# Performance work log

Measured on AMD Instinct MI355X. Metric: run time of the kernel, lower is better.

Reference implementation:

```python
import jax, jax.numpy as jnp
import numpy as np

T, N, H = 256, 64, 512
DT, GAMMA, EPS = 0.01, 1.0, 1.0

def setup_inputs() -> dict:
    key = jax.random.key(0)
    ks = jax.random.split(key, 6)
    s = 1.0 / np.sqrt(H)  # keep recurrent dynamics stable
    return {
        "x": jax.random.normal(ks[0], (T, N, H), jnp.float32),
        "connection_matrix": (jax.random.uniform(ks[1], (N, N)) < 0.5).astype(jnp.float32),
        "W_h": jax.random.normal(ks[2], (N, H, H), jnp.float32) * s,
        "W_x": jax.random.normal(ks[3], (N, H, H), jnp.float32) * s,
        "b": jax.random.normal(ks[4], (N, H), jnp.float32) * 0.1,
        "initial_states": jnp.zeros((N, 2, H), jnp.float32),
    }

def reference(x, connection_matrix, W_h, W_x, b, initial_states):
    # x: (T, N, H); states: (N, 2, H) with states[:,0] = h_y (the archetype output)
    def step(carry, x_t):
        states, outs = carry
        # message passing: mix previous outputs through the connection matrix,
        # then gate with the external input (elementwise)
        new_ins = (connection_matrix @ outs) * x_t                      # (N, H)
        hy, hz = states[:, 0], states[:, 1]
        # batched RON cell over all N archetypes
        pre = (jnp.einsum('nij,nj->ni', W_h, hy)
               + jnp.einsum('nij,nj->ni', W_x, new_ins) + b)            # (N, H)
        hz_n = hz + DT * (jnp.tanh(pre) - GAMMA * hy - EPS * hz)
        hy_n = hy + DT * hz_n
        new_states = jnp.stack([hy_n, hz_n], axis=1)                    # (N, 2, H)
        return (new_states, hy_n), (new_states, new_ins)

    init_outs = jnp.zeros_like(x[0])  # initial_outs=None path in the original
    _, (states_seq, ins_seq) = jax.lax.scan(step, (initial_states, init_outs), x)
    # original prepends the initial state and x[0] to the returned lists
    states_all = jnp.concatenate([initial_states[None], states_seq], axis=0)  # (T+1, N, 2, H)
    ins_all = jnp.concatenate([x[:1], ins_seq], axis=0)                       # (T+1, N, H)
    return states_all, ins_all
```

## Files before the change

kernel.cpp:

```cpp
#include <hip/hip_runtime.h>
#include <hip/hip_cooperative_groups.h>

namespace cg = cooperative_groups;

constexpr int   T_     = 256;
constexpr int   N_     = 64;
constexpr int   H_     = 512;
constexpr float DT_    = 0.01f;
constexpr float GAMMA_ = 1.0f;
constexpr float EPS_   = 1.0f;

constexpr int GRID  = 1024;
constexpr int BLOCK = 256;
constexpr int WGPN  = GRID / N_;
constexpr int ROWS  = H_ / WGPN;
constexpr int RPW   = ROWS / 4;
constexpr int LROWS = 16;

__global__ __launch_bounds__(BLOCK, 4)
void archetypes_persistent(const float* __restrict__ x,
                           const float* __restrict__ conn,
                           const float* __restrict__ W_h,
                           const float* __restrict__ W_x,
                           const float* __restrict__ bias,
                           const float* __restrict__ init_states,
                           float* __restrict__ out)
{
    cg::grid_group grid = cg::this_grid();

    const int tid  = threadIdx.x;
    const int wg   = blockIdx.x;
    const int n    = wg / WGPN;
    const int q    = wg % WGPN;
    const int lane = tid & 63;
    const int wave = tid >> 6;

    float* states_all = out;
    float* ins_all    = out + (size_t)(T_ + 1) * N_ * 2 * H_;

    __shared__ float s_hy[H_];
    __shared__ float s_ins[H_];
    __shared__ float s_pre[ROWS];
    __shared__ float s_conn[N_];
    __shared__ float s_bias[ROWS];
    __shared__ float s_wx[LROWS][H_];

    const float4* Wh4 = (const float4*)(W_h + ((size_t)n * H_ + q * ROWS) * H_);
    const float4* Wx4 = (const float4*)(W_x + ((size_t)n * H_ + q * ROWS) * H_);
    float4 wh_reg[RPW][2];
    #pragma unroll
    for (int j = 0; j < RPW; ++j) {
        const int r_l = wave + 4 * j;
        #pragma unroll
        for (int k = 0; k < 2; ++k)
            wh_reg[j][k] = Wh4[r_l * (H_ / 4) + k * 64 + lane];
    }
    {
        float4* dst = (float4*)&s_wx[0][0];
        for (int idx = tid; idx < LROWS * H_ / 4; idx += BLOCK)
            dst[idx] = Wx4[idx];
    }
    if (tid < N_)   s_conn[tid] = conn[n * N_ + tid];
    if (tid < ROWS) s_bias[tid] = bias[n * H_ + q * ROWS + tid];

    for (int idx = wg * BLOCK + tid; idx < N_ * 2 * H_; idx += GRID * BLOCK)
        states_all[idx] = init_states[idx];
    for (int idx = wg * BLOCK + tid; idx < N_ * H_; idx += GRID * BLOCK)
        ins_all[idx] = x[idx];

    grid.sync();

    for (int t = 0; t < T_; ++t) {
        const float* st_t = states_all + (size_t)t * N_ * 2 * H_;

        {
            const int h0 = tid, h1 = tid + 256;
            float i0 = 0.f, i1 = 0.f;
            if (t > 0) {
                const float* xr = x + (size_t)t * N_ * H_ + n * H_;
                float a0 = 0.f, a1 = 0.f;
                #pragma unroll 8
                for (int m = 0; m < N_; ++m) {
                    const float c = s_conn[m];
                    a0 += c * st_t[m * 2 * H_ + h0];
                    a1 += c * st_t[m * 2 * H_ + h1];
                }
                i0 = a0 * xr[h0];
                i1 = a1 * xr[h1];
            }
            s_ins[h0] = i0;
            s_ins[h1] = i1;
            s_hy[h0] = st_t[n * 2 * H_ + h0];
            s_hy[h1] = st_t[n * 2 * H_ + h1];
            float* insd = ins_all + (size_t)(t + 1) * N_ * H_ + n * H_;
            if (h0 / ROWS == q) insd[h0] = i0;
            if (h1 / ROWS == q) insd[h1] = i1;
        }
        __syncthreads();

        {
            const float4* vh = (const float4*)s_hy;
            const float4* vi = (const float4*)s_ins;
            const float4 v0 = vh[lane], v1 = vh[64 + lane];
            const float4 u0 = vi[lane], u1 = vi[64 + lane];
            #pragma unroll
            for (int j = 0; j < RPW; ++j) {
                const int r_l = wave + 4 * j;
                float4 wx0, wx1;
                if (j < 4) {
                    const float4* lx = (const float4*)&s_wx[r_l][0];
                    wx0 = lx[lane];
                    wx1 = lx[64 + lane];
                } else {
                    wx0 = Wx4[r_l * (H_ / 4) + lane];
                    wx1 = Wx4[r_l * (H_ / 4) + 64 + lane];
                }
                float acc = 0.f;
                acc += wh_reg[j][0].x * v0.x + wh_reg[j][0].y * v0.y +
                       wh_reg[j][0].z * v0.z + wh_reg[j][0].w * v0.w;
                acc += wx0.x * u0.x + wx0.y * u0.y + wx0.z * u0.z + wx0.w * u0.w;
                acc += wh_reg[j][1].x * v1.x + wh_reg[j][1].y * v1.y +
                       wh_reg[j][1].z * v1.z + wh_reg[j][1].w * v1.w;
                acc += wx1.x * u1.x + wx1.y * u1.y + wx1.z * u1.z + wx1.w * u1.w;
                #pragma unroll
                for (int off = 32; off; off >>= 1)
                    acc += __shfl_xor(acc, off);
                if (lane == 0) s_pre[r_l] = acc;
            }
        }
        __syncthreads();

        if (tid < ROWS) {
            const int i   = q * ROWS + tid;
            const float pre  = s_pre[tid] + s_bias[tid];
            const float hy   = st_t[n * 2 * H_ + i];
            const float hz   = st_t[n * 2 * H_ + H_ + i];
            const float th   = tanhf(pre);
            const float hz_n = hz + DT_ * (th - GAMMA_ * hy - EPS_ * hz);
            const float hy_n = hy + DT_ * hz_n;
            float* st1 = states_all + (size_t)(t + 1) * N_ * 2 * H_ + n * 2 * H_;
            st1[i]      = hy_n;
            st1[H_ + i] = hz_n;
        }

        grid.sync();
    }
}

__global__ __launch_bounds__(BLOCK)
void archetypes_init(const float* __restrict__ x,
                     const float* __restrict__ init_states,
                     float* __restrict__ out)
{
    float* states_all = out;
    float* ins_all    = out + (size_t)(T_ + 1) * N_ * 2 * H_;
    const int idx = blockIdx.x * BLOCK + threadIdx.x;
    if (idx < N_ * 2 * H_) states_all[idx] = init_states[idx];
    if (idx < N_ * H_)     ins_all[idx]    = x[idx];
}

__global__ __launch_bounds__(BLOCK)
void archetypes_step(int t,
                     const float* __restrict__ x,
                     const float* __restrict__ conn,
                     const float* __restrict__ W_h,
                     const float* __restrict__ W_x,
                     const float* __restrict__ bias,
                     float* __restrict__ out)
{
    const int tid  = threadIdx.x;
    const int wg   = blockIdx.x;
    const int n    = wg / WGPN;
    const int q    = wg % WGPN;
    const int lane = tid & 63;
    const int wave = tid >> 6;

    float* states_all = out;
    float* ins_all    = out + (size_t)(T_ + 1) * N_ * 2 * H_;

    __shared__ float s_hy[H_];
    __shared__ float s_ins[H_];
    __shared__ float s_pre[ROWS];
    __shared__ float s_conn[N_];
    __shared__ float s_bias[ROWS];

    if (tid < N_)   s_conn[tid] = conn[n * N_ + tid];
    if (tid < ROWS) s_bias[tid] = bias[n * H_ + q * ROWS + tid];
    __syncthreads();

    const float* st_t = states_all + (size_t)t * N_ * 2 * H_;
    {
        const int h0 = tid, h1 = tid + 256;
        float i0 = 0.f, i1 = 0.f;
        if (t > 0) {
            const float* xr = x + (size_t)t * N_ * H_ + n * H_;
            float a0 = 0.f, a1 = 0.f;
            #pragma unroll 8
            for (int m = 0; m < N_; ++m) {
                const float c = s_conn[m];
                a0 += c * st_t[m * 2 * H_ + h0];
                a1 += c * st_t[m * 2 * H_ + h1];
            }
            i0 = a0 * xr[h0];
            i1 = a1 * xr[h1];
        }
        s_ins[h0] = i0;
        s_ins[h1] = i1;
        s_hy[h0] = st_t[n * 2 * H_ + h0];
        s_hy[h1] = st_t[n * 2 * H_ + h1];
        float* insd = ins_all + (size_t)(t + 1) * N_ * H_ + n * H_;
        if (h0 / ROWS == q) insd[h0] = i0;
        if (h1 / ROWS == q) insd[h1] = i1;
    }
    __syncthreads();
    {
        const float4* vh = (const float4*)s_hy;
        const float4* vi = (const float4*)s_ins;
        const float4* Wh4 = (const float4*)(W_h + ((size_t)n * H_ + q * ROWS) * H_);
        const float4* Wx4 = (const float4*)(W_x + ((size_t)n * H_ + q * ROWS) * H_);
        const float4 v0 = vh[lane], v1 = vh[64 + lane];
        const float4 u0 = vi[lane], u1 = vi[64 + lane];
        #pragma unroll
        for (int j = 0; j < RPW; ++j) {
            const int r_l = wave + 4 * j;
            const float4 a0 = Wh4[r_l * (H_ / 4) + lane];
            const float4 a1 = Wh4[r_l * (H_ / 4) + 64 + lane];
            const float4 wx0 = Wx4[r_l * (H_ / 4) + lane];
            const float4 wx1 = Wx4[r_l * (H_ / 4) + 64 + lane];
            float acc = 0.f;
            acc += a0.x * v0.x + a0.y * v0.y + a0.z * v0.z + a0.w * v0.w;
            acc += wx0.x * u0.x + wx0.y * u0.y + wx0.z * u0.z + wx0.w * u0.w;
            acc += a1.x * v1.x + a1.y * v1.y + a1.z * v1.z + a1.w * v1.w;
            acc += wx1.x * u1.x + wx1.y * u1.y + wx1.z * u1.z + wx1.w * u1.w;
            #pragma unroll
            for (int off = 32; off; off >>= 1)
                acc += __shfl_xor(acc, off);
            if (lane == 0) s_pre[r_l] = acc;
        }
    }
    __syncthreads();
    if (tid < ROWS) {
        const int i   = q * ROWS + tid;
        const float pre  = s_pre[tid] + s_bias[tid];
        const float hy   = st_t[n * 2 * H_ + i];
        const float hz   = st_t[n * 2 * H_ + H_ + i];
        const float th   = tanhf(pre);
        const float hz_n = hz + DT_ * (th - GAMMA_ * hy - EPS_ * hz);
        const float hy_n = hy + DT_ * hz_n;
        float* st1 = states_all + (size_t)(t + 1) * N_ * 2 * H_ + n * 2 * H_;
        st1[i]      = hy_n;
        st1[H_ + i] = hz_n;
    }
}

extern "C" void kernel_launch(void* const* d_in, const int* in_sizes, int n_in,
                              void* d_out, int out_size, void* d_ws, size_t ws_size,
                              hipStream_t stream) {
    const float* x     = (const float*)d_in[0];
    const float* conn  = (const float*)d_in[1];
    const float* W_h   = (const float*)d_in[2];
    const float* W_x   = (const float*)d_in[3];
    const float* bias  = (const float*)d_in[4];
    const float* inits = (const float*)d_in[5];
    float*       outp  = (float*)d_out;

    int perCU = 0;
    (void)hipOccupancyMaxActiveBlocksPerMultiprocessor(
        &perCU, (const void*)archetypes_persistent, BLOCK, 0);
    const bool coop_ok = (perCU * 256 >= GRID);

    if (coop_ok) {
        void* args[] = {(void*)&x, (void*)&conn, (void*)&W_h, (void*)&W_x,
                        (void*)&bias, (void*)&inits, (void*)&outp};
        hipLaunchCooperativeKernel((void*)archetypes_persistent,
                                   dim3(GRID), dim3(BLOCK), args, 0, stream);
    } else {
        archetypes_init<<<dim3((N_ * 2 * H_ + BLOCK - 1) / BLOCK), dim3(BLOCK),
                          0, stream>>>(x, inits, outp);
        for (int t = 0; t < T_; ++t)
            archetypes_step<<<dim3(GRID), dim3(BLOCK), 0, stream>>>(
                t, x, conn, W_h, W_x, bias, outp);
    }
}
```

Before: 6.792 ms.

## Replace cooperative grid sync with atomic barrier and regroup into 1024-thread blocks

Replaces the cooperative-groups grid.sync with a hand-written atomic counter/generation barrier on a workspace buffer, reset by a memset before launch. The grid shrinks to 256 blocks of 1024 threads, so fewer workgroups take part in each of the 256 per-step barriers. Part of each block's W_x slice moves into registers and the rest into a larger LDS tile, removing per-step global reloads of W_x. hy is also read from shared memory in the update stage. The trade-offs are heavy register and LDS pressure (128KB of shared memory, plus 96 weight registers per thread under strict launch bounds), which risks spills. Forward progress of the custom barrier also depends on all 256 blocks being co-resident.

```diff
diff --git a/kernel.cpp b/kernel.cpp
--- a/kernel.cpp
+++ b/kernel.cpp
@@ -1,21 +1,37 @@
 #include <hip/hip_runtime.h>
-#include <hip/hip_cooperative_groups.h>
-
-namespace cg = cooperative_groups;
-
-constexpr int   T_     = 256;
-constexpr int   N_     = 64;
-constexpr int   H_     = 512;
-constexpr float DT_    = 0.01f;
-constexpr float GAMMA_ = 1.0f;
-constexpr float EPS_   = 1.0f;
-
-constexpr int GRID  = 1024;
-constexpr int BLOCK = 256;
+
+constexpr int   T_ = 256, N_ = 64, H_ = 512;
+constexpr float DT_ = 0.01f, GAMMA_ = 1.0f, EPS_ = 1.0f;
+
+constexpr int GRID  = 256;
+constexpr int BLOCK = 1024;
 constexpr int WGPN  = GRID / N_;
 constexpr int ROWS  = H_ / WGPN;
-constexpr int RPW   = ROWS / 4;
-constexpr int LROWS = 16;
+constexpr int WAVES = BLOCK / 64;
+constexpr int RPW   = ROWS / WAVES;
+constexpr int LJ    = 4;
+
+__device__ __forceinline__ void grid_barrier(unsigned* cnt, unsigned* gen,
+                                             unsigned target) {
+    __syncthreads();
+    if (threadIdx.x == 0) {
+        __threadfence();
+        unsigned prev = __hip_atomic_fetch_add(cnt, 1u, __ATOMIC_ACQ_REL,
+                                               __HIP_MEMORY_SCOPE_AGENT);
+        if (prev == (unsigned)GRID - 1u) {
+            __hip_atomic_store(cnt, 0u, __ATOMIC_RELAXED,
+                               __HIP_MEMORY_SCOPE_AGENT);
+            __hip_atomic_fetch_add(gen, 1u, __ATOMIC_RELEASE,
+                                   __HIP_MEMORY_SCOPE_AGENT);
+        } else {
+            while (__hip_atomic_load(gen, __ATOMIC_ACQUIRE,
+                                     __HIP_MEMORY_SCOPE_AGENT) < target)
+                __builtin_amdgcn_s_sleep(1);
+        }
+    }
+    __syncthreads();
+    __threadfence();
+}
 
 __global__ __launch_bounds__(BLOCK, 4)
 void archetypes_persistent(const float* __restrict__ x,
@@ -24,10 +40,9 @@
                            const float* __restrict__ W_x,
                            const float* __restrict__ bias,
                            const float* __restrict__ init_states,
-                           float* __restrict__ out)
+                           float* __restrict__ out,
+                           unsigned* __restrict__ bar)
 {
-    cg::grid_group grid = cg::this_grid();
-
     const int tid  = threadIdx.x;
     const int wg   = blockIdx.x;
     const int n    = wg / WGPN;
@@ -38,26 +53,33 @@
     float* states_all = out;
     float* ins_all    = out + (size_t)(T_ + 1) * N_ * 2 * H_;
 
+    __shared__ float s_wx[LJ * WAVES][H_];
     __shared__ float s_hy[H_];
     __shared__ float s_ins[H_];
     __shared__ float s_pre[ROWS];
     __shared__ float s_conn[N_];
     __shared__ float s_bias[ROWS];
-    __shared__ float s_wx[LROWS][H_];
 
     const float4* Wh4 = (const float4*)(W_h + ((size_t)n * H_ + q * ROWS) * H_);
     const float4* Wx4 = (const float4*)(W_x + ((size_t)n * H_ + q * ROWS) * H_);
+
     float4 wh_reg[RPW][2];
+    float4 wx_reg[RPW - LJ][2];
     #pragma unroll
     for (int j = 0; j < RPW; ++j) {
-        const int r_l = wave + 4 * j;
-        #pragma unroll
-        for (int k = 0; k < 2; ++k)
-            wh_reg[j][k] = Wh4[r_l * (H_ / 4) + k * 64 + lane];
+        const int r_l = wave + WAVES * j;
+        wh_reg[j][0] = Wh4[r_l * (H_ / 4) + lane];
+        wh_reg[j][1] = Wh4[r_l * (H_ / 4) + 64 + lane];
+    }
+    #pragma unroll
+    for (int j = LJ; j < RPW; ++j) {
+        const int r_l = wave + WAVES * j;
+        wx_reg[j - LJ][0] = Wx4[r_l * (H_ / 4) + lane];
+        wx_reg[j - LJ][1] = Wx4[r_l * (H_ / 4) + 64 + lane];
     }
     {
         float4* dst = (float4*)&s_wx[0][0];
-        for (int idx = tid; idx < LROWS * H_ / 4; idx += BLOCK)
+        for (int idx = tid; idx < LJ * WAVES * (H_ / 4); idx += BLOCK)
             dst[idx] = Wx4[idx];
     }
     if (tid < N_)   s_conn[tid] = conn[n * N_ + tid];
@@ -68,33 +90,32 @@
     for (int idx = wg * BLOCK + tid; idx < N_ * H_; idx += GRID * BLOCK)
         ins_all[idx] = x[idx];
 
-    grid.sync();
+    unsigned* cnt = bar;
+    unsigned* gen = bar + 1;
+    unsigned bt = 0;
+
+    grid_barrier(cnt, gen, ++bt);
+
+    const int half = tid >> 9;
+    const int h    = tid & (H_ - 1);
 
     for (int t = 0; t < T_; ++t) {
         const float* st_t = states_all + (size_t)t * N_ * 2 * H_;
 
-        {
-            const int h0 = tid, h1 = tid + 256;
-            float i0 = 0.f, i1 = 0.f;
+        if (!half) {
+            float i0 = 0.f;
             if (t > 0) {
-                const float* xr = x + (size_t)t * N_ * H_ + n * H_;
-                float a0 = 0.f, a1 = 0.f;
+                float a = 0.f;
                 #pragma unroll 8
-                for (int m = 0; m < N_; ++m) {
-                    const float c = s_conn[m];
-                    a0 += c * st_t[m * 2 * H_ + h0];
-                    a1 += c * st_t[m * 2 * H_ + h1];
-                }
-                i0 = a0 * xr[h0];
-                i1 = a1 * xr[h1];
+                for (int m = 0; m < N_; ++m)
+                    a += s_conn[m] * st_t[m * 2 * H_ + h];
+                i0 = a * x[(size_t)t * N_ * H_ + n * H_ + h];
             }
-            s_ins[h0] = i0;
-            s_ins[h1] = i1;
-            s_hy[h0] = st_t[n * 2 * H_ + h0];
-            s_hy[h1] = st_t[n * 2 * H_ + h1];
+            s_ins[h] = i0;
             float* insd = ins_all + (size_t)(t + 1) * N_ * H_ + n * H_;
-            if (h0 / ROWS == q) insd[h0] = i0;
-            if (h1 / ROWS == q) insd[h1] = i1;
+            if (h / ROWS == q) insd[h] = i0;
+        } else {
+            s_hy[h] = st_t[n * 2 * H_ + h];
         }
         __syncthreads();
 
@@ -105,15 +126,15 @@
             const float4 u0 = vi[lane], u1 = vi[64 + lane];
             #pragma unroll
             for (int j = 0; j < RPW; ++j) {
-                const int r_l = wave + 4 * j;
+                const int r_l = wave + WAVES * j;
                 float4 wx0, wx1;
-                if (j < 4) {
+                if (j < LJ) {
                     const float4* lx = (const float4*)&s_wx[r_l][0];
                     wx0 = lx[lane];
                     wx1 = lx[64 + lane];
                 } else {
-                    wx0 = Wx4[r_l * (H_ / 4) + lane];
-                    wx1 = Wx4[r_l * (H_ / 4) + 64 + lane];
+                    wx0 = wx_reg[j - LJ][0];
+                    wx1 = wx_reg[j - LJ][1];
                 }
                 float acc = 0.f;
                 acc += wh_reg[j][0].x * v0.x + wh_reg[j][0].y * v0.y +
@@ -131,9 +152,9 @@
         __syncthreads();
 
         if (tid < ROWS) {
-            const int i   = q * ROWS + tid;
+            const int i    = q * ROWS + tid;
             const float pre  = s_pre[tid] + s_bias[tid];
-            const float hy   = st_t[n * 2 * H_ + i];
+            const float hy   = s_hy[i];
             const float hz   = st_t[n * 2 * H_ + H_ + i];
             const float th   = tanhf(pre);
             const float hz_n = hz + DT_ * (th - GAMMA_ * hy - EPS_ * hz);
@@ -143,23 +164,25 @@
             st1[H_ + i] = hz_n;
         }
 
-        grid.sync();
-    }
-}
-
-__global__ __launch_bounds__(BLOCK)
+        grid_barrier(cnt, gen, ++bt);
+    }
+}
+
+constexpr int FGRID = 1024, FBLOCK = 256, FWGPN = 16, FROWS = 32, FRPW = 8;
+
+__global__ __launch_bounds__(FBLOCK)
 void archetypes_init(const float* __restrict__ x,
                      const float* __restrict__ init_states,
                      float* __restrict__ out)
 {
     float* states_all = out;
     float* ins_all    = out + (size_t)(T_ + 1) * N_ * 2 * H_;
-    const int idx = blockIdx.x * BLOCK + threadIdx.x;
+    const int idx = blockIdx.x * FBLOCK + threadIdx.x;
     if (idx < N_ * 2 * H_) states_all[idx] = init_states[idx];
     if (idx < N_ * H_)     ins_all[idx]    = x[idx];
 }
 
-__global__ __launch_bounds__(BLOCK)
+__global__ __launch_bounds__(FBLOCK)
 void archetypes_step(int t,
                      const float* __restrict__ x,
                      const float* __restrict__ conn,
@@ -170,8 +193,8 @@
 {
     const int tid  = threadIdx.x;
     const int wg   = blockIdx.x;
-    const int n    = wg / WGPN;
-    const int q    = wg % WGPN;
+    const int n    = wg / FWGPN;
+    const int q    = wg % FWGPN;
     const int lane = tid & 63;
     const int wave = tid >> 6;
 
@@ -180,12 +203,12 @@
 
     __shared__ float s_hy[H_];
     __shared__ float s_ins[H_];
-    __shared__ float s_pre[ROWS];
+    __shared__ float s_pre[FROWS];
     __shared__ float s_conn[N_];
-    __shared__ float s_bias[ROWS];
-
-    if (tid < N_)   s_conn[tid] = conn[n * N_ + tid];
-    if (tid < ROWS) s_bias[tid] = bias[n * H_ + q * ROWS + tid];
+    __shared__ float s_bias[FROWS];
+
+    if (tid < N_)    s_conn[tid] = conn[n * N_ + tid];
+    if (tid < FROWS) s_bias[tid] = bias[n * H_ + q * FROWS + tid];
     __syncthreads();
 
     const float* st_t = states_all + (size_t)t * N_ * 2 * H_;
@@ -209,19 +232,19 @@
         s_hy[h0] = st_t[n * 2 * H_ + h0];
         s_hy[h1] = st_t[n * 2 * H_ + h1];
         float* insd = ins_all + (size_t)(t + 1) * N_ * H_ + n * H_;
-        if (h0 / ROWS == q) insd[h0] = i0;
-        if (h1 / ROWS == q) insd[h1] = i1;
+        if (h0 / FROWS == q) insd[h0] = i0;
+        if (h1 / FROWS == q) insd[h1] = i1;
     }
     __syncthreads();
     {
         const float4* vh = (const float4*)s_hy;
         const float4* vi = (const float4*)s_ins;
-        const float4* Wh4 = (const float4*)(W_h + ((size_t)n * H_ + q * ROWS) * H_);
-        const float4* Wx4 = (const float4*)(W_x + ((size_t)n * H_ + q * ROWS) * H_);
+        const float4* Wh4 = (const float4*)(W_h + ((size_t)n * H_ + q * FROWS) * H_);
+        const float4* Wx4 = (const float4*)(W_x + ((size_t)n * H_ + q * FROWS) * H_);
         const float4 v0 = vh[lane], v1 = vh[64 + lane];
         const float4 u0 = vi[lane], u1 = vi[64 + lane];
         #pragma unroll
-        for (int j = 0; j < RPW; ++j) {
+        for (int j = 0; j < FRPW; ++j) {
             const int r_l = wave + 4 * j;
             const float4 a0 = Wh4[r_l * (H_ / 4) + lane];
             const float4 a1 = Wh4[r_l * (H_ / 4) + 64 + lane];
@@ -239,8 +262,8 @@
         }
     }
     __syncthreads();
-    if (tid < ROWS) {
-        const int i   = q * ROWS + tid;
+    if (tid < FROWS) {
+        const int i   = q * FROWS + tid;
         const float pre  = s_pre[tid] + s_bias[tid];
         const float hy   = st_t[n * 2 * H_ + i];
         const float hz   = st_t[n * 2 * H_ + H_ + i];
@@ -263,6 +286,7 @@
     const float* bias  = (const float*)d_in[4];
     const float* inits = (const float*)d_in[5];
     float*       outp  = (float*)d_out;
+    unsigned*    bar   = (unsigned*)d_ws;
 
     int perCU = 0;
     (void)hipOccupancyMaxActiveBlocksPerMultiprocessor(
@@ -270,15 +294,16 @@
     const bool coop_ok = (perCU * 256 >= GRID);
 
     if (coop_ok) {
+        hipMemsetAsync(bar, 0, 2 * sizeof(unsigned), stream);
         void* args[] = {(void*)&x, (void*)&conn, (void*)&W_h, (void*)&W_x,
-                        (void*)&bias, (void*)&inits, (void*)&outp};
+                        (void*)&bias, (void*)&inits, (void*)&outp, (void*)&bar};
         hipLaunchCooperativeKernel((void*)archetypes_persistent,
                                    dim3(GRID), dim3(BLOCK), args, 0, stream);
     } else {
-        archetypes_init<<<dim3((N_ * 2 * H_ + BLOCK - 1) / BLOCK), dim3(BLOCK),
+        archetypes_init<<<dim3((N_ * 2 * H_ + FBLOCK - 1) / FBLOCK), dim3(FBLOCK),
                           0, stream>>>(x, inits, outp);
         for (int t = 0; t < T_; ++t)
-            archetypes_step<<<dim3(GRID), dim3(BLOCK), 0, stream>>>(
+            archetypes_step<<<dim3(FGRID), dim3(FBLOCK), 0, stream>>>(
                 t, x, conn, W_h, W_x, bias, outp);
     }
 }
```

Result: no change. 6.730 ms (-0.9%).
